# Kernel optimization log

Hardware: AMD Instinct MI355X
Metric: run time of the kernel (lower is better)

The kernel has to match this reference:

```python
import jax, jax.numpy as jnp
import numpy as np

S_STA = 32          # s_sta_dim
N_TS = 4            # n_timesteps
NUM_FREQ = 4        # NeRF PE octaves -> 2 + 2*2*4 = 18 PE channels
EPS_NORM = 1e-12    # torch F.normalize default eps


def pos_enc_concat(v):
    # v: (B, C, H, W) -> concat NeRF positional encoding of pixel grid on channel dim
    B, C, H, W = v.shape
    ys = jnp.linspace(-1.0, 1.0, H)
    xs = jnp.linspace(-1.0, 1.0, W)
    coords = jnp.stack(jnp.meshgrid(ys, xs, indexing='ij'), axis=0)  # (2, H, W)
    feats = [coords]
    for i in range(NUM_FREQ):
        f = (2.0 ** i) * jnp.pi * coords
        feats.append(jnp.sin(f))
        feats.append(jnp.cos(f))
    pe = jnp.concatenate(feats, axis=0).astype(v.dtype)              # (18, H, W)
    pe = jnp.broadcast_to(pe[None], (B,) + pe.shape)
    return jnp.concatenate([v, pe], axis=1)


def setup_inputs() -> dict:
    key = jax.random.key(0)
    k1, k2, k3 = jax.random.split(key, 3)
    ch = 128
    x = jax.random.normal(k1, (4, 4, 12, ch, 24, 24), dtype=jnp.float32)
    Wv = jax.random.normal(k2, (ch, ch), dtype=jnp.float32) / np.float32(np.sqrt(ch))
    bv = jax.random.normal(k3, (ch,), dtype=jnp.float32) * 0.01
    return {"x": x, "Wv": Wv, "bv": bv, "temp": 1}


def reference(x, Wv, bv, temp):
    bs, N, T, ch, h, w = x.shape
    BN, hw = bs * N, h * w
    scale = ch ** (-0.5)
    xf = x.reshape(BN, T, ch, h, w)

    # F.normalize(p=2, dim=-3): L2-normalize over channel dim
    nrm = jnp.sqrt(jnp.sum(xf * xf, axis=2, keepdims=True))
    x_att = xf / jnp.maximum(nrm, EPS_NORM)

    qs = x_att[:, 1:].reshape(BN * (T - 1), ch, hw)
    ks = x_att[:, :-1].reshape(BN * (T - 1), ch, hw)
    energy = jnp.einsum('bcn,bcm->bnm', qs, ks).reshape(BN, T - 1, hw, hw) * scale
    attn = jax.nn.softmax(energy / temp, axis=-1)       # (BN, T-1, hw, hw)

    # to_v: 1x1 conv then NeRF PE concat
    v = jnp.einsum('oc,btchw->btohw', Wv, xf) + bv[None, None, :, None, None]
    v = pos_enc_concat(v.reshape(BN * T, ch, h, w))     # (BN*T, ch+18, h, w)
    vs_pe = v.reshape(BN, T, -1, hw)                    # (BN, T, C_v, hw)

    Tp = T - N_TS + 1
    acc = vs_pe[:, :Tp, S_STA:]                         # (BN, Tp, C_v-S_STA, hw)
    for t in range(N_TS - 1):                           # small fixed recurrence depth
        cs = vs_pe[:, t + 1:t + 1 + Tp, S_STA:]
        ca = attn[:, t:t + Tp]
        prop = jnp.einsum('btcm,btnm->btcn', acc, ca)
        acc = jnp.concatenate([cs, prop], axis=2)
    return acc
```

## Files before the change

kernel.cpp:

```cpp
#include <hip/hip_runtime.h>
#include <math.h>

#define BN 16
#define T 12
#define CH 128
#define HW 576
#define TM1 11
#define TP 9
#define CCS 114

typedef __attribute__((ext_vector_type(8))) short bf16x8;
typedef __attribute__((ext_vector_type(4))) float floatx4;

__device__ inline float b2f(unsigned short u) {
    unsigned int v = ((unsigned int)u) << 16;
    return __builtin_bit_cast(float, v);
}
__device__ inline unsigned short f2b(float f) {
    unsigned int v = __builtin_bit_cast(unsigned int, f);
    unsigned int r = (v + 0x7FFFu + ((v >> 16) & 1u)) >> 16;
    return (unsigned short)r;
}

__device__ __forceinline__ void async_copy16(void* lds, const void* g) {
    __builtin_amdgcn_global_load_lds(
        (const __attribute__((address_space(1))) unsigned int*)g,
        (__attribute__((address_space(3))) unsigned int*)lds,
        16, 0, 0);
}

__global__ __launch_bounds__(256) void k_norm_t(const float* __restrict__ x,
                                                unsigned short* __restrict__ xT) {
    int bt = blockIdx.x / 9;
    int p0 = (blockIdx.x % 9) * 64;
    int t = threadIdx.x;
    int lane = t & 63, wave = t >> 6;
    int pq = t & 15;
    int cg = t >> 4;
    const float* src = x + (size_t)bt * CH * HW + (size_t)(cg * 8) * HW + p0 + pq * 4;

    floatx4 v[8];
    float s0 = 0.f, s1 = 0.f, s2 = 0.f, s3 = 0.f;
#pragma unroll
    for (int j = 0; j < 8; j++) {
        v[j] = *(const floatx4*)(src + (size_t)j * HW);
        s0 = fmaf(v[j][0], v[j][0], s0);
        s1 = fmaf(v[j][1], v[j][1], s1);
        s2 = fmaf(v[j][2], v[j][2], s2);
        s3 = fmaf(v[j][3], v[j][3], s3);
    }
#pragma unroll
    for (int m = 16; m < 64; m <<= 1) {
        s0 += __shfl_xor(s0, m);
        s1 += __shfl_xor(s1, m);
        s2 += __shfl_xor(s2, m);
        s3 += __shfl_xor(s3, m);
    }
    __shared__ float smP[4][16][4];
    __shared__ float smI[64];
    if (lane < 16) {
        smP[wave][lane][0] = s0; smP[wave][lane][1] = s1;
        smP[wave][lane][2] = s2; smP[wave][lane][3] = s3;
    }
    __syncthreads();
    if (t < 64) {
        int q = t >> 2, k = t & 3;
        float tot = smP[0][q][k] + smP[1][q][k] + smP[2][q][k] + smP[3][q][k];
        smI[t] = 1.0f / fmaxf(sqrtf(tot), 1e-12f);
    }
    __syncthreads();
    unsigned short* dst = xT + ((size_t)bt * HW + p0 + pq * 4) * CH + cg * 8;
#pragma unroll
    for (int k = 0; k < 4; k++) {
        float inv = smI[pq * 4 + k];
        union { unsigned short u[8]; uint4 q4; } pk;
#pragma unroll
        for (int j = 0; j < 8; j++) pk.u[j] = f2b(v[j][k] * inv);
        *(uint4*)(dst + (size_t)k * CH) = pk.q4;
    }
}

__global__ __launch_bounds__(256) void k_energy(const unsigned short* __restrict__ xT,
                                                unsigned short* __restrict__ attn,
                                                const int* __restrict__ temp) {
    int z = blockIdx.z; int b = z / TM1; int ti = z % TM1;
    const unsigned short* Q = xT + (size_t)(b * T + ti + 1) * HW * CH;
    const unsigned short* K = xT + (size_t)(b * T + ti) * HW * CH;
    unsigned short* E = attn + (size_t)z * HW * HW;
    int n0 = blockIdx.y * 96, m0 = blockIdx.x * 96;

    int lane = threadIdx.x & 63;
    int wave = threadIdx.x >> 6;
    int wy = wave >> 1, wx = wave & 1;
    int fr = lane & 15;
    int koff = (lane >> 4) * 8;

    const unsigned short* aptr[3];
    const unsigned short* bptr[3];
#pragma unroll
    for (int i = 0; i < 3; i++) {
        aptr[i] = Q + (size_t)(n0 + wy * 48 + i * 16 + fr) * CH + koff;
        bptr[i] = K + (size_t)(m0 + wx * 48 + i * 16 + fr) * CH + koff;
    }
    floatx4 acc[3][3] = {};
#pragma unroll
    for (int k0 = 0; k0 < CH; k0 += 32) {
        bf16x8 af[3], bfr[3];
#pragma unroll
        for (int i = 0; i < 3; i++) { af[i] = *(const bf16x8*)(aptr[i]); aptr[i] += 32; }
#pragma unroll
        for (int j = 0; j < 3; j++) { bfr[j] = *(const bf16x8*)(bptr[j]); bptr[j] += 32; }
#pragma unroll
        for (int i = 0; i < 3; i++)
#pragma unroll
            for (int j = 0; j < 3; j++)
                acc[i][j] = __builtin_amdgcn_mfma_f32_16x16x32_bf16(af[i], bfr[j], acc[i][j], 0, 0, 0);
    }
    float sc = 0.08838834764831845f / (float)temp[0];
    int crow = (lane >> 4) * 4, ccol = lane & 15;
#pragma unroll
    for (int i = 0; i < 3; i++) {
#pragma unroll
        for (int reg = 0; reg < 4; reg++) {
            int n = n0 + wy * 48 + i * 16 + crow + reg;
#pragma unroll
            for (int j = 0; j < 3; j++) {
                int m = m0 + wx * 48 + j * 16 + ccol;
                E[(size_t)n * HW + m] = f2b(acc[i][j][reg] * sc);
            }
        }
    }
}

__global__ __launch_bounds__(256) void k_softmax(unsigned short* __restrict__ attn) {
    int row = blockIdx.x * 4 + (threadIdx.x >> 6);
    int lane = threadIdx.x & 63;
    unsigned short* a = attn + (size_t)row * HW + lane;

    float v[9];
#pragma unroll
    for (int j = 0; j < 9; j++) v[j] = b2f(a[64 * j]);

    float m = v[0];
#pragma unroll
    for (int j = 1; j < 9; j++) m = fmaxf(m, v[j]);
#pragma unroll
    for (int i = 1; i < 64; i <<= 1) m = fmaxf(m, __shfl_xor(m, i));

    float s = 0.f;
#pragma unroll
    for (int j = 0; j < 9; j++) { v[j] = __expf(v[j] - m); s += v[j]; }
#pragma unroll
    for (int i = 1; i < 64; i <<= 1) s += __shfl_xor(s, i);

    float inv = 1.0f / s;
#pragma unroll
    for (int j = 0; j < 9; j++) a[64 * j] = f2b(v[j] * inv);
}

__global__ __launch_bounds__(256) void k_vgemm(const float* __restrict__ x,
                                               const float* __restrict__ Wv,
                                               const float* __restrict__ bv,
                                               unsigned short* __restrict__ cs16,
                                               float* __restrict__ out) {
    int bt = blockIdx.z;
    int b = bt / T, t = bt % T;
    const float* X = x + (size_t)bt * CH * HW;
    unsigned short* C16 = cs16 + (size_t)bt * CCS * HW;
    float* O = (t >= 3) ? out + (size_t)(b * TP + t - 3) * 456 * HW : nullptr;
    int m0 = blockIdx.y * 64, n0 = blockIdx.x * 64;
    __shared__ float As[16][66];
    __shared__ float Bs[16][66];
    int tid = threadIdx.x;
    int kq = tid % 16, lr = tid / 16;
    int tx = tid % 16, ty = tid / 16;
    int lp = tid % 64, lc = tid / 64;
    float acc[4][4] = {};
    for (int c0 = 0; c0 < CH; c0 += 16) {
#pragma unroll
        for (int i = 0; i < 4; i++) {
            int r = m0 + lr + 16 * i;
            As[kq][lr + 16 * i] = (r < 96) ? Wv[(size_t)(32 + r) * CH + c0 + kq] : 0.f;
        }
#pragma unroll
        for (int i = 0; i < 4; i++) {
            int c = lc + 4 * i;
            Bs[c][lp] = X[(size_t)(c0 + c) * HW + n0 + lp];
        }
        __syncthreads();
#pragma unroll
        for (int kk = 0; kk < 16; kk++) {
            float2 a01 = *(const float2*)&As[kk][ty * 4];
            float2 a23 = *(const float2*)&As[kk][ty * 4 + 2];
            float2 b01 = *(const float2*)&Bs[kk][tx * 4];
            float2 b23 = *(const float2*)&Bs[kk][tx * 4 + 2];
            float av[4] = {a01.x, a01.y, a23.x, a23.y};
            float bw[4] = {b01.x, b01.y, b23.x, b23.y};
#pragma unroll
            for (int i = 0; i < 4; i++)
#pragma unroll
                for (int j = 0; j < 4; j++)
                    acc[i][j] = fmaf(av[i], bw[j], acc[i][j]);
        }
        __syncthreads();
    }
#pragma unroll
    for (int i = 0; i < 4; i++) {
        int r = m0 + ty * 4 + i;
        if (r < 96) {
            float bb = bv[32 + r];
            floatx4 o;
            o[0] = acc[i][0] + bb; o[1] = acc[i][1] + bb;
            o[2] = acc[i][2] + bb; o[3] = acc[i][3] + bb;
            union { unsigned short u[4]; uint2 v; } pk;
            pk.u[0] = f2b(o[0]); pk.u[1] = f2b(o[1]); pk.u[2] = f2b(o[2]); pk.u[3] = f2b(o[3]);
            *(uint2*)(C16 + (size_t)r * HW + n0 + tx * 4) = pk.v;
            if (O) __builtin_nontemporal_store(o, (floatx4*)(O + (size_t)r * HW + n0 + tx * 4));
        }
    }
}

__global__ __launch_bounds__(576) void k_pe(unsigned short* __restrict__ cs16,
                                            float* __restrict__ out) {
    int bt = blockIdx.x;
    int b = bt / T, t = bt % T;
    int p = threadIdx.x;
    unsigned short* C16 = cs16 + ((size_t)bt * CCS + 96) * HW + p;
    float* O = (t >= 3) ? out + ((size_t)(b * TP + t - 3) * 456 + 96) * HW + p : nullptr;
    int iy = p / 24, ix = p % 24;
    float y = -1.f + 2.f * (float)iy / 23.f;
    float xx = -1.f + 2.f * (float)ix / 23.f;
    float vals[18];
    vals[0] = y; vals[1] = xx;
    const float PI = 3.14159265358979323846f;
#pragma unroll
    for (int i = 0; i < 4; i++) {
        float k = (float)(1 << i) * PI;
        float fy = k * y, fx = k * xx;
        vals[2 + 4 * i + 0] = sinf(fy);
        vals[2 + 4 * i + 1] = sinf(fx);
        vals[2 + 4 * i + 2] = cosf(fy);
        vals[2 + 4 * i + 3] = cosf(fx);
    }
#pragma unroll
    for (int c = 0; c < 18; c++) {
        C16[(size_t)c * HW] = f2b(vals[c]);
        if (O) __builtin_nontemporal_store(vals[c], O + (size_t)c * HW);
    }
}

template<int M_, bool F32OUT>
__global__ __launch_bounds__(256) void k_stage(const unsigned short* __restrict__ cs16,
                                               const unsigned short* __restrict__ prop_in,
                                               const unsigned short* __restrict__ attn,
                                               float* __restrict__ dst_f32,
                                               unsigned short* __restrict__ dst_b16,
                                               int tshift, int prop_ch,
                                               int dst_stride_ch, int dst_ch_off) {
    constexpr int MT = (M_ + 127) / 128;
    constexpr int WPZ = MT * 6;
    constexpr int BUFSZ = 28672;

    int nwg = gridDim.x;
    int wg = (blockIdx.x & 7) * (nwg >> 3) + (blockIdx.x >> 3);
    int z = wg / WPZ;
    int rem = wg % WPZ;
    int mt = rem / 6, nt = rem % 6;
    int m0 = mt * 128, n0 = nt * 96;

    int b = z / TP, tp = z % TP;
    const unsigned short* csz = cs16 + (size_t)((b * T + tp + tshift) * CCS) * HW;
    const unsigned short* prz = prop_in ? prop_in + (size_t)z * prop_ch * HW : csz;
    const unsigned short* Bm = attn + (size_t)(b * TM1 + tp + tshift) * HW * HW;

    __shared__ uint4 smq[2 * BUFSZ / 16];
    char* smc = (char*)smq;

    int tid = threadIdx.x;
    int lane = tid & 63, wave = tid >> 6;
    int wm = wave >> 1, wn = wave & 1;
    int fr = lane & 15, hi = lane >> 4;

    int cp = tid & 7;
    int rloc = tid >> 3;
    const unsigned short* srcA[4];
#pragma unroll
    for (int i = 0; i < 4; i++) {
        int r = i * 32 + rloc;
        int rg = m0 + r;
        const unsigned short* p;
        if (rg < CCS) p = csz + (size_t)rg * HW;
        else if (rg < M_) p = prz + (size_t)(rg - CCS) * HW;
        else p = csz;
        srcA[i] = p + ((cp ^ (r & 7)) << 3);
    }
    const unsigned short* srcB[3];
#pragma unroll
    for (int i = 0; i < 3; i++) {
        int r = i * 32 + rloc;
        srcB[i] = Bm + (size_t)(n0 + r) * HW + ((cp ^ (r & 7)) << 3);
    }

    int arow[4], brow[3];
#pragma unroll
    for (int i = 0; i < 4; i++) arow[i] = (wm * 64 + i * 16 + fr) * 128;
#pragma unroll
    for (int j = 0; j < 3; j++) brow[j] = (wn * 48 + j * 16 + fr) * 128;
    int xr = fr & 7;

    floatx4 acc[4][3] = {};
    int buf = 0;

    {
        char* base = smc;
        int wo = wave * 1024;
#pragma unroll
        for (int i = 0; i < 4; i++) async_copy16(base + i * 4096 + wo, srcA[i]);
#pragma unroll
        for (int i = 0; i < 3; i++) async_copy16(base + 16384 + i * 4096 + wo, srcB[i]);
    }
    __syncthreads();

    for (int t = 0; t < 9; ++t) {
        if (t < 8) {
            char* nb = smc + (buf ^ 1) * BUFSZ;
            int wo = wave * 1024;
            int ko = (t + 1) * 64;
#pragma unroll
            for (int i = 0; i < 4; i++) async_copy16(nb + i * 4096 + wo, srcA[i] + ko);
#pragma unroll
            for (int i = 0; i < 3; i++) async_copy16(nb + 16384 + i * 4096 + wo, srcB[i] + ko);
        }
        char* base = smc + buf * BUFSZ;
#pragma unroll
        for (int s = 0; s < 2; ++s) {
            int coff = ((s * 4 + hi) ^ xr) << 4;
            bf16x8 af[4], bfr[3];
#pragma unroll
            for (int i = 0; i < 4; i++) af[i] = *(const bf16x8*)(base + arow[i] + coff);
#pragma unroll
            for (int j = 0; j < 3; j++) bfr[j] = *(const bf16x8*)(base + 16384 + brow[j] + coff);
#pragma unroll
            for (int i = 0; i < 4; i++)
#pragma unroll
                for (int j = 0; j < 3; j++)
                    acc[i][j] = __builtin_amdgcn_mfma_f32_16x16x32_bf16(af[i], bfr[j], acc[i][j], 0, 0, 0);
        }
        __syncthreads();
        buf ^= 1;
    }

    int crow = hi * 4, ccol = fr;
#pragma unroll
    for (int i = 0; i < 4; i++) {
#pragma unroll
        for (int reg = 0; reg < 4; reg++) {
            int r = m0 + wm * 64 + i * 16 + crow + reg;
            if (r < M_) {
#pragma unroll
                for (int j = 0; j < 3; j++) {
                    int n = n0 + wn * 48 + j * 16 + ccol;
                    size_t idx = ((size_t)z * dst_stride_ch + dst_ch_off + r) * HW + n;
                    if (F32OUT) __builtin_nontemporal_store(acc[i][j][reg], dst_f32 + idx);
                    else dst_b16[idx] = f2b(acc[i][j][reg]);
                }
            }
        }
    }
}

extern "C" void kernel_launch(void* const* d_in, const int* in_sizes, int n_in,
                              void* d_out, int out_size, void* d_ws, size_t ws_size,
                              hipStream_t stream) {
    const float* x  = (const float*)d_in[0];
    const float* Wv = (const float*)d_in[1];
    const float* bv = (const float*)d_in[2];
    const int* temp = (const int*)d_in[3];
    float* out = (float*)d_out;

    char* w = (char*)d_ws;
    unsigned short* xT     = (unsigned short*)w;
    w += (size_t)192 * HW * CH * 2;
    unsigned short* attn16 = (unsigned short*)w;
    w += (size_t)176 * HW * HW * 2;
    unsigned short* cs16   = (unsigned short*)w;
    w += (size_t)192 * CCS * HW * 2;
    unsigned short* p1     = (unsigned short*)w;
    w += (size_t)144 * CCS * HW * 2;
    unsigned short* p2     = (unsigned short*)w;

    k_norm_t<<<192 * 9, 256, 0, stream>>>(x, xT);
    k_energy<<<dim3(6, 6, 176), 256, 0, stream>>>(xT, attn16, temp);
    k_softmax<<<BN * TM1 * HW / 4, 256, 0, stream>>>(attn16);
    k_vgemm<<<dim3(9, 2, 192), 256, 0, stream>>>(x, Wv, bv, cs16, out);
    k_pe<<<192, 576, 0, stream>>>(cs16, out);
    k_stage<114, false><<<dim3(864),  256, 0, stream>>>(cs16, nullptr, attn16, nullptr, p1, 0, 0, 114, 0);
    k_stage<228, false><<<dim3(1728), 256, 0, stream>>>(cs16, p1, attn16, nullptr, p2, 1, 114, 228, 0);
    k_stage<342, true ><<<dim3(2592), 256, 0, stream>>>(cs16, p2, attn16, out, nullptr, 2, 228, 456, 114);
}
```

Measured before the change: 516.2 us.

## Fuse softmax into energy GEMM with full-row tiles per workgroup

Replaces the separate energy GEMM and softmax kernels with one kernel where each workgroup computes 32 full attention rows across 4 waves. It does the row max/sum reduction via shuffles and shared memory, then writes normalized bf16 probabilities once. This removes a full read-modify-write pass over the large attention matrix and one launch. Blocks are also remapped with an XCD-style swizzle. The cost is higher register pressure from 18 accumulators per wave and different tile shapes for the GEMM.

```diff
diff --git a/kernel.cpp b/kernel.cpp
--- a/kernel.cpp
+++ b/kernel.cpp
@@ -80,82 +80,115 @@
     }
 }
 
-__global__ __launch_bounds__(256) void k_energy(const unsigned short* __restrict__ xT,
-                                                unsigned short* __restrict__ attn,
-                                                const int* __restrict__ temp) {
-    int z = blockIdx.z; int b = z / TM1; int ti = z % TM1;
+__global__ __launch_bounds__(256, 2) void k_energysm(const unsigned short* __restrict__ xT,
+                                                     unsigned short* __restrict__ attn,
+                                                     const int* __restrict__ temp) {
+    int nwg = gridDim.x;
+    int wg = (blockIdx.x & 7) * (nwg >> 3) + (blockIdx.x >> 3);
+    int z = wg / 18, nt = wg % 18;
+    int b = z / TM1, ti = z % TM1;
     const unsigned short* Q = xT + (size_t)(b * T + ti + 1) * HW * CH;
     const unsigned short* K = xT + (size_t)(b * T + ti) * HW * CH;
-    unsigned short* E = attn + (size_t)z * HW * HW;
-    int n0 = blockIdx.y * 96, m0 = blockIdx.x * 96;
-
-    int lane = threadIdx.x & 63;
-    int wave = threadIdx.x >> 6;
-    int wy = wave >> 1, wx = wave & 1;
-    int fr = lane & 15;
-    int koff = (lane >> 4) * 8;
-
-    const unsigned short* aptr[3];
-    const unsigned short* bptr[3];
-#pragma unroll
-    for (int i = 0; i < 3; i++) {
-        aptr[i] = Q + (size_t)(n0 + wy * 48 + i * 16 + fr) * CH + koff;
-        bptr[i] = K + (size_t)(m0 + wx * 48 + i * 16 + fr) * CH + koff;
-    }
-    floatx4 acc[3][3] = {};
-#pragma unroll
-    for (int k0 = 0; k0 < CH; k0 += 32) {
-        bf16x8 af[3], bfr[3];
-#pragma unroll
-        for (int i = 0; i < 3; i++) { af[i] = *(const bf16x8*)(aptr[i]); aptr[i] += 32; }
-#pragma unroll
-        for (int j = 0; j < 3; j++) { bfr[j] = *(const bf16x8*)(bptr[j]); bptr[j] += 32; }
-#pragma unroll
-        for (int i = 0; i < 3; i++)
-#pragma unroll
-            for (int j = 0; j < 3; j++)
-                acc[i][j] = __builtin_amdgcn_mfma_f32_16x16x32_bf16(af[i], bfr[j], acc[i][j], 0, 0, 0);
-    }
+    unsigned short* A = attn + (size_t)z * HW * HW;
+    int n0 = nt * 32;
+
+    int lane = threadIdx.x & 63, wave = threadIdx.x >> 6;
+    int fr = lane & 15, hi = lane >> 4;
+    int koff = hi * 8;
+    int m0 = wave * 144;
+
+    bf16x8 af[4][2];
+#pragma unroll
+    for (int k0 = 0; k0 < 4; k0++)
+#pragma unroll
+        for (int fi = 0; fi < 2; fi++)
+            af[k0][fi] = *(const bf16x8*)(Q + (size_t)(n0 + fi * 16 + fr) * CH + k0 * 32 + koff);
+
+    floatx4 acc[2][9] = {};
+#pragma unroll
+    for (int k0 = 0; k0 < 4; k0++) {
+        bf16x8 bfr[9];
+#pragma unroll
+        for (int j = 0; j < 9; j++)
+            bfr[j] = *(const bf16x8*)(K + (size_t)(m0 + j * 16 + fr) * CH + k0 * 32 + koff);
+#pragma unroll
+        for (int fi = 0; fi < 2; fi++)
+#pragma unroll
+            for (int j = 0; j < 9; j++)
+                acc[fi][j] = __builtin_amdgcn_mfma_f32_16x16x32_bf16(af[k0][fi], bfr[j], acc[fi][j], 0, 0, 0);
+    }
+
+    __shared__ float smMax[4][32];
+    __shared__ float smSum[4][32];
     float sc = 0.08838834764831845f / (float)temp[0];
-    int crow = (lane >> 4) * 4, ccol = lane & 15;
-#pragma unroll
-    for (int i = 0; i < 3; i++) {
+
+    float pm[2][4];
+#pragma unroll
+    for (int fi = 0; fi < 2; fi++)
 #pragma unroll
         for (int reg = 0; reg < 4; reg++) {
-            int n = n0 + wy * 48 + i * 16 + crow + reg;
-#pragma unroll
-            for (int j = 0; j < 3; j++) {
-                int m = m0 + wx * 48 + j * 16 + ccol;
-                E[(size_t)n * HW + m] = f2b(acc[i][j][reg] * sc);
+            float m = acc[fi][0][reg];
+#pragma unroll
+            for (int j = 1; j < 9; j++) m = fmaxf(m, acc[fi][j][reg]);
+#pragma unroll
+            for (int msk = 1; msk < 16; msk <<= 1) m = fmaxf(m, __shfl_xor(m, msk));
+            pm[fi][reg] = m;
+        }
+    if (fr == 0) {
+#pragma unroll
+        for (int fi = 0; fi < 2; fi++)
+#pragma unroll
+            for (int reg = 0; reg < 4; reg++)
+                smMax[wave][fi * 16 + hi * 4 + reg] = pm[fi][reg];
+    }
+    __syncthreads();
+
+    float rmax[2][4];
+#pragma unroll
+    for (int fi = 0; fi < 2; fi++)
+#pragma unroll
+        for (int reg = 0; reg < 4; reg++) {
+            int row = fi * 16 + hi * 4 + reg;
+            rmax[fi][reg] = fmaxf(fmaxf(smMax[0][row], smMax[1][row]),
+                                  fmaxf(smMax[2][row], smMax[3][row]));
+        }
+
+    float ps[2][4];
+#pragma unroll
+    for (int fi = 0; fi < 2; fi++)
+#pragma unroll
+        for (int reg = 0; reg < 4; reg++) {
+            float s = 0.f;
+#pragma unroll
+            for (int j = 0; j < 9; j++) {
+                float e = __expf(sc * (acc[fi][j][reg] - rmax[fi][reg]));
+                acc[fi][j][reg] = e;
+                s += e;
             }
-        }
-    }
-}
-
-__global__ __launch_bounds__(256) void k_softmax(unsigned short* __restrict__ attn) {
-    int row = blockIdx.x * 4 + (threadIdx.x >> 6);
-    int lane = threadIdx.x & 63;
-    unsigned short* a = attn + (size_t)row * HW + lane;
-
-    float v[9];
-#pragma unroll
-    for (int j = 0; j < 9; j++) v[j] = b2f(a[64 * j]);
-
-    float m = v[0];
-#pragma unroll
-    for (int j = 1; j < 9; j++) m = fmaxf(m, v[j]);
-#pragma unroll
-    for (int i = 1; i < 64; i <<= 1) m = fmaxf(m, __shfl_xor(m, i));
-
-    float s = 0.f;
-#pragma unroll
-    for (int j = 0; j < 9; j++) { v[j] = __expf(v[j] - m); s += v[j]; }
-#pragma unroll
-    for (int i = 1; i < 64; i <<= 1) s += __shfl_xor(s, i);
-
-    float inv = 1.0f / s;
-#pragma unroll
-    for (int j = 0; j < 9; j++) a[64 * j] = f2b(v[j] * inv);
+#pragma unroll
+            for (int msk = 1; msk < 16; msk <<= 1) s += __shfl_xor(s, msk);
+            ps[fi][reg] = s;
+        }
+    if (fr == 0) {
+#pragma unroll
+        for (int fi = 0; fi < 2; fi++)
+#pragma unroll
+            for (int reg = 0; reg < 4; reg++)
+                smSum[wave][fi * 16 + hi * 4 + reg] = ps[fi][reg];
+    }
+    __syncthreads();
+
+#pragma unroll
+    for (int fi = 0; fi < 2; fi++)
+#pragma unroll
+        for (int reg = 0; reg < 4; reg++) {
+            int row = fi * 16 + hi * 4 + reg;
+            float inv = 1.0f / (smSum[0][row] + smSum[1][row] + smSum[2][row] + smSum[3][row]);
+            int n = n0 + row;
+#pragma unroll
+            for (int j = 0; j < 9; j++)
+                A[(size_t)n * HW + m0 + j * 16 + fr] = f2b(acc[fi][j][reg] * inv);
+        }
 }
 
 __global__ __launch_bounds__(256) void k_vgemm(const float* __restrict__ x,
@@ -390,8 +423,7 @@
     unsigned short* p2     = (unsigned short*)w;
 
     k_norm_t<<<192 * 9, 256, 0, stream>>>(x, xT);
-    k_energy<<<dim3(6, 6, 176), 256, 0, stream>>>(xT, attn16, temp);
-    k_softmax<<<BN * TM1 * HW / 4, 256, 0, stream>>>(attn16);
+    k_energysm<<<dim3(3168), 256, 0, stream>>>(xT, attn16, temp);
     k_vgemm<<<dim3(9, 2, 192), 256, 0, stream>>>(x, Wv, bv, cs16, out);
     k_pe<<<192, 576, 0, stream>>>(cs16, out);
     k_stage<114, false><<<dim3(864),  256, 0, stream>>>(cs16, nullptr, attn16, nullptr, p1, 0, 0, 114, 0);
```

New measurement: 486.0 us. 1.06x faster.
